# Performance work log

Hardware: AMD Instinct MI355X
Metric: run time of the kernel (lower is better)

## Reference

```python
import jax, jax.numpy as jnp
import numpy as np

N_QUBITS = 8
DEPTH = 1
INPUT_DIM = 64
HIDDEN = 8  # must equal N_QUBITS
SEQ = 64
BATCH = 256


def _apply_rx(state, wire, ang):
    # state: (B, 2, 2, ..., 2) with wire w on axis 1+w; ang: (B,) angles
    n = state.ndim - 1
    st = jnp.moveaxis(state, 1 + wire, -1)
    a0, a1 = st[..., 0], st[..., 1]
    half = ang * 0.5
    c = jnp.cos(half).reshape((-1,) + (1,) * (n - 1))
    s = jnp.sin(half).reshape((-1,) + (1,) * (n - 1))
    new = jnp.stack([c * a0 - 1j * s * a1, c * a1 - 1j * s * a0], axis=-1)
    return jnp.moveaxis(new, -1, 1 + wire)


def _apply_cnot(state, cw, tw):
    st = jnp.moveaxis(state, (1 + cw, 1 + tw), (-2, -1))
    st = st.at[..., 1, :].set(st[..., 1, ::-1])  # flip target where control=1
    return jnp.moveaxis(st, (-2, -1), (1 + cw, 1 + tw))


def qgate(theta, qparams):
    # theta: (B, n) data-dependent RX angles; qparams: (n,) trainable RX angles
    B, n = theta.shape
    state = jnp.zeros((B,) + (2,) * n, dtype=jnp.complex64)
    state = state.at[(slice(None),) + (0,) * n].set(1.0 + 0.0j)  # |0...0>
    for w in range(n):
        state = _apply_rx(state, w, theta[:, w])
    for w in range(n - 1):
        state = _apply_cnot(state, w, w + 1)
    for w in range(n):
        state = _apply_rx(state, w, jnp.broadcast_to(qparams[w], (B,)))
    probs = jnp.abs(state) ** 2  # (B, 2, ..., 2)
    expz = []
    for w in range(n):
        pw = probs.sum(axis=tuple(a for a in range(1, n + 1) if a != 1 + w))  # (B, 2)
        expz.append(pw[:, 0] - pw[:, 1])  # <Z_w>
    return jnp.stack(expz, axis=1)  # (B, n)


def setup_inputs() -> dict:
    key = jax.random.key(0)
    ks = jax.random.split(key, 13)
    d_in = INPUT_DIM + HIDDEN
    d_out = N_QUBITS * DEPTH
    sc = 1.0 / np.sqrt(d_in)
    inp = {"inputs": jax.random.normal(ks[0], (SEQ, BATCH, INPUT_DIM), dtype=jnp.float32)}
    names = ["f", "i", "g", "o"]
    for j, nm in enumerate(names):
        inp["W" + nm] = jax.random.uniform(ks[1 + 3 * j], (d_out, d_in), minval=-sc, maxval=sc, dtype=jnp.float32)
        inp["b" + nm] = jax.random.uniform(ks[2 + 3 * j], (d_out,), minval=-sc, maxval=sc, dtype=jnp.float32)
        inp["q" + nm] = jax.random.normal(ks[3 + 3 * j], (d_out,), dtype=jnp.float32)
    return inp


def reference(inputs, Wf, bf, qf, Wi, bi, qi, Wg, bg, qg, Wo, bo, qo):
    B = inputs.shape[1]
    hx0 = jnp.zeros((B, HIDDEN), dtype=inputs.dtype)
    cx0 = jnp.zeros((B, HIDDEN), dtype=inputs.dtype)

    def step(carry, x_t):
        hx, cx = carry
        comb = jnp.concatenate([x_t, hx], axis=1)  # (B, input+hidden)
        f = jax.nn.sigmoid(qgate(comb @ Wf.T + bf, qf))
        i_ = jax.nn.sigmoid(qgate(comb @ Wi.T + bi, qi))
        g = jnp.tanh(qgate(comb @ Wg.T + bg, qg))
        o = jax.nn.sigmoid(qgate(comb @ Wo.T + bo, qo))
        cx = f * cx + i_ * g
        hx = o * jnp.tanh(cx)
        return (hx, cx), hx

    (hx, cx), outputs = jax.lax.scan(step, (hx0, cx0), inputs)
    return outputs, (hx, cx)
```

## Files before the change

### kernel.cpp

```cpp
#include <hip/hip_runtime.h>
#include <hip/hip_bf16.h>

__device__ float g_pre_static[8 * 1024 * 1024];

__device__ __forceinline__ float rcp_(float x)   { return __builtin_amdgcn_rcpf(x); }
__device__ __forceinline__ float sigm_f(float x) { return rcp_(1.0f + __expf(-x)); }
__device__ __forceinline__ float tanh_f(float x) { return 1.0f - 2.0f*rcp_(__expf(2.0f*x) + 1.0f); }
__device__ __forceinline__ float sigm(float x)  { return 1.0f/(1.0f + __expf(-x)); }
__device__ __forceinline__ float tanh_(float x) { float e = __expf(2.0f*x); return (e-1.0f)/(e+1.0f); }

template<int IDD>
__global__ __launch_bounds__(64) void k_pre8(
    const float* __restrict__ x_,
    const float* __restrict__ W0, const float* __restrict__ b0p,
    const float* __restrict__ W1, const float* __restrict__ b1p,
    const float* __restrict__ W2, const float* __restrict__ b2p,
    const float* __restrict__ W3, const float* __restrict__ b3p,
    float* __restrict__ pre, int S, int B)
{
    constexpr int DIN = IDD + 8;
    __shared__ float wsh[32 * IDD];
    __shared__ float sb32[32];
    const int t   = blockIdx.x;
    const int tid = threadIdx.x;
    const long b  = (long)blockIdx.y * 64 + tid;
    const float* Wp[4] = {W0, W1, W2, W3};
    const float* bp[4] = {b0p, b1p, b2p, b3p};

    #pragma unroll
    for (int it = 0; it < (32*IDD)/64; ++it) {
        int idx = it*64 + tid;
        int gw = idx / IDD, k = idx % IDD;
        wsh[idx] = Wp[gw >> 3][(gw & 7)*DIN + k];
    }
    if (tid < 32) sb32[tid] = bp[tid >> 3][tid & 7];
    __syncthreads();

    if (b >= B) return;
    float xr[IDD];
    const float4* xv = (const float4*)(x_ + ((long)t*B + b)*IDD);
    #pragma unroll
    for (int i = 0; i < IDD/4; ++i) {
        float4 v = xv[i];
        xr[4*i] = v.x; xr[4*i+1] = v.y; xr[4*i+2] = v.z; xr[4*i+3] = v.w;
    }

    float acc[32];
    #pragma unroll
    for (int gw = 0; gw < 32; ++gw) {
        float a = sb32[gw];
        const float4* wr = (const float4*)&wsh[gw*IDD];
        #pragma unroll
        for (int k4 = 0; k4 < IDD/4; ++k4) {
            float4 wv = wr[k4];
            a += xr[4*k4]*wv.x + xr[4*k4+1]*wv.y + xr[4*k4+2]*wv.z + xr[4*k4+3]*wv.w;
        }
        acc[gw] = a;
    }
    float4* op = (float4*)(pre + ((long)t*B + b)*32);
    #pragma unroll
    for (int i = 0; i < 8; ++i)
        op[i] = make_float4(acc[4*i], acc[4*i+1], acc[4*i+2], acc[4*i+3]);
}

__global__ __launch_bounds__(256) void k_pre_gen(
    const float* __restrict__ x_,
    const float* W0, const float* b0p,
    const float* W1, const float* b1p,
    const float* W2, const float* b2p,
    const float* W3, const float* b3p,
    float* __restrict__ pre,
    int S, int B, int ID, int H, int SP)
{
    extern __shared__ float lds[];
    const int dIn  = ID + H;
    const int dInP = dIn + 1;
    float* xs    = lds;
    float* wsh   = lds + 64*SP;
    float* sbias = wsh + 4*H*dInP;
    const int t   = blockIdx.x;
    const int tid = threadIdx.x;
    const int bl  = tid & 63;
    const int q   = tid >> 6;
    const int b0  = blockIdx.y * 64;
    const float* Wp[4] = {W0, W1, W2, W3};
    const float* bp[4] = {b0p, b1p, b2p, b3p};

    for (int g = 0; g < 4; ++g)
        for (int idx = tid; idx < H*dIn; idx += 256) {
            int w = idx / dIn, k = idx - w*dIn;
            wsh[(g*H + w)*dInP + k] = Wp[g][idx];
        }
    for (int idx = tid; idx < 4*H; idx += 256)
        sbias[idx] = bp[idx / H][idx % H];

    {
        int total = 64 * ID;
        for (int i = tid; i < total; i += 256) {
            int r = i / ID, c = i - r*ID;
            long bb = (long)b0 + r; if (bb >= B) bb = B - 1;
            xs[r*SP + c] = x_[((long)t*B + bb)*ID + c];
        }
    }
    __syncthreads();

    const int b = b0 + bl;
    if (b < B) {
        const float* xrow = &xs[bl*SP];
        float* orow = pre + (((long)t*B + b)*4 + q)*H;
        for (int w = 0; w < H; ++w) {
            float acc = sbias[q*H + w];
            const float* wrow = &wsh[(q*H + w)*dInP];
            for (int k = 0; k < ID; ++k) acc += xrow[k] * wrow[k];
            orow[w] = acc;
        }
    }
}

__global__ __launch_bounds__(64) void k_rec8(
    const float* __restrict__ W0, const float* __restrict__ q0,
    const float* __restrict__ W1, const float* __restrict__ q1,
    const float* __restrict__ W2, const float* __restrict__ q2,
    const float* __restrict__ W3, const float* __restrict__ q3,
    const float* __restrict__ pre,
    float* __restrict__ out, int S, int B, int ID)
{
    const int dIn  = ID + 8;
    const int lane = threadIdx.x;
    const int gw   = lane & 31;
    const int g    = gw >> 3;
    const int w    = gw & 7;
    const int b    = blockIdx.x*2 + (lane >> 5);
    const int bs   = (b < B) ? b : (B - 1);
    const float* Wp[4] = {W0, W1, W2, W3};
    const float* qp[4] = {q0, q1, q2, q3};

    float wr[8];
    #pragma unroll
    for (int j = 0; j < 8; ++j) wr[j] = Wp[g][(long)w*dIn + ID + j];
    const float qv   = qp[g][w];
    const float mult = (w < 7) ? __cosf(qv) : 1.0f;
    const float qadd = (w == 7) ? qv : 0.0f;
    const float ascl = (g == 2) ? 2.0f : 1.0f;
    const float aoff = (g == 2) ? -1.0f : 0.0f;

    int oct = lane & 56;
    int srcw[8];
    #pragma unroll
    for (int j = 0; j < 8; ++j) srcw[j] = oct | j;
    int srcg[4];
    #pragma unroll
    for (int G = 0; G < 4; ++G) srcg[G] = (lane & 32) | (G << 3) | w;

    float cxw = 0.0f, hxw = 0.0f;
    float hxj[8];
    #pragma unroll
    for (int j = 0; j < 8; ++j) hxj[j] = 0.0f;

    const float* base = pre + (long)bs*32 + gw;
    const long  tstep = (long)B*32;

    float pf[4];
    #pragma unroll
    for (int d = 0; d < 4; ++d) {
        int tt = (d < S) ? d : (S - 1);
        pf[d] = base[(long)tt*tstep];
    }

    for (int t0 = 0; t0 < S; t0 += 4) {
        #pragma unroll
        for (int d = 0; d < 4; ++d) {
            const int t = t0 + d;
            if (t < S) {
                float pcur = pf[d];
                int tn = t + 4; if (tn >= S) tn = S - 1;
                pf[d] = base[(long)tn*tstep];

                float th = pcur;
                #pragma unroll
                for (int j = 0; j < 8; ++j) th = fmaf(wr[j], hxj[j], th);
                float c = __cosf(th + qadd);

                float cj[8];
                #pragma unroll
                for (int j = 0; j < 8; ++j) cj[j] = __shfl(c, srcw[j], 64);
                float P = cj[0];
                #pragma unroll
                for (int j = 1; j < 8; ++j) P *= (j <= w) ? cj[j] : 1.0f;

                float act = ascl * sigm_f(ascl * (mult * P)) + aoff;

                float fv = __shfl(act, srcg[0], 64);
                float iv = __shfl(act, srcg[1], 64);
                float gv = __shfl(act, srcg[2], 64);
                float ov = __shfl(act, srcg[3], 64);

                cxw = fv*cxw + iv*gv;
                hxw = ov * tanh_f(cxw);

                if (g == 0 && b < B) out[((long)t*B + b)*8 + w] = hxw;

                #pragma unroll
                for (int j = 0; j < 8; ++j) hxj[j] = __shfl(hxw, srcw[j], 64);
            }
        }
    }

    if (g == 0 && b < B) {
        out[((long)S*B + b)*8 + w]     = hxw;
        out[((long)S*B + B + b)*8 + w] = cxw;
    }
}

__global__ __launch_bounds__(64) void k_rec_g(
    const float* __restrict__ pre,
    const float* W0, const float* q0,
    const float* W1, const float* q1,
    const float* W2, const float* q2,
    const float* W3, const float* q3,
    float* __restrict__ out, int S, int B, int ID, int H)
{
    __shared__ float sWh[4*32*32];
    __shared__ float scq[4*32];
    const int dIn = ID + H;
    const int tid = threadIdx.x;
    const int b   = blockIdx.x*64 + tid;
    const float* Wp[4] = {W0, W1, W2, W3};
    const float* qp[4] = {q0, q1, q2, q3};

    for (int idx = tid; idx < 4*H*H; idx += 64) {
        int g = idx / (H*H), r = idx % (H*H);
        int w = r / H, j = r % H;
        sWh[(g*H + w)*H + j] = Wp[g][(long)w*dIn + ID + j];
    }
    for (int idx = tid; idx < 4*H; idx += 64) {
        int g = idx / H, w = idx % H;
        float qv = qp[g][w];
        scq[idx] = (w < H-1) ? __cosf(qv) : qv;
    }
    __syncthreads();
    if (b >= B) return;

    float hx[32], cx[32], gate[4][32], th[32];
    for (int w = 0; w < H; ++w) { hx[w] = 0.0f; cx[w] = 0.0f; }

    for (int t = 0; t < S; ++t) {
        const float* pt = pre + ((long)t*B + b)*4*H;
        for (int g = 0; g < 4; ++g) {
            for (int w = 0; w < H; ++w) {
                float a = pt[g*H + w];
                const float* wrp = &sWh[(g*H + w)*H];
                for (int j = 0; j < H; ++j) a += wrp[j]*hx[j];
                th[w] = a;
            }
            float cum = 1.0f;
            for (int w = 0; w < H-1; ++w) {
                cum *= __cosf(th[w]);
                gate[g][w] = scq[g*H + w] * cum;
            }
            gate[g][H-1] = cum * __cosf(th[H-1] + scq[g*H + H-1]);
        }
        float* orow = out + ((long)t*B + b)*H;
        for (int w = 0; w < H; ++w) {
            float fv = sigm (gate[0][w]);
            float iv = sigm (gate[1][w]);
            float gv = tanh_(gate[2][w]);
            float ov = sigm (gate[3][w]);
            cx[w] = fv*cx[w] + iv*gv;
            hx[w] = ov*tanh_(cx[w]);
            orow[w] = hx[w];
        }
    }
    float* oh = out + ((long)S*B + b)*H;
    float* oc = out + ((long)S*B + B + b)*H;
    for (int w = 0; w < H; ++w) { oh[w] = hx[w]; oc[w] = cx[w]; }
}

static bool derive(long sz[13], long osz, long& S, long& B, long& ID, long& H) {
    H = sz[3];
    long dIn = (H > 0) ? sz[1] / H : 0;
    ID = dIn - H;
    long TB = (ID > 0) ? sz[0] / ID : 0;
    B = (H > 0) ? (osz / H - TB) / 2 : 0;
    S = (B > 0) ? TB / B : 0;
    return (H >= 1 && H <= 32 && ID >= 1 && B >= 1 && S >= 1 &&
            S*B == TB && (S*B + 2*B)*H == osz &&
            dIn*H == sz[1] && TB*ID == sz[0]);
}

extern "C" void kernel_launch(void* const* d_in, const int* in_sizes, int n_in,
                              void* d_out, int out_size, void* d_ws, size_t ws_size,
                              hipStream_t stream) {
    const float* x  = (const float*)d_in[0];
    const float* Wf = (const float*)d_in[1];  const float* bfv = (const float*)d_in[2];  const float* qf = (const float*)d_in[3];
    const float* Wi = (const float*)d_in[4];  const float* biv = (const float*)d_in[5];  const float* qi = (const float*)d_in[6];
    const float* Wg = (const float*)d_in[7];  const float* bgv = (const float*)d_in[8];  const float* qg = (const float*)d_in[9];
    const float* Wo = (const float*)d_in[10]; const float* bov = (const float*)d_in[11]; const float* qo = (const float*)d_in[12];
    float* out = (float*)d_out;

    long S = 0, B = 0, ID = 0, H = 0;
    bool ok = false;
    for (int scale : {1, 4, 2}) {
        long sz[13];
        for (int i = 0; i < 13; ++i) sz[i] = (long)in_sizes[i] / scale;
        long osz = (long)out_size / scale;
        if (derive(sz, osz, S, B, ID, H)) { ok = true; break; }
    }
    if (!ok) { H = 8; ID = 64; B = 256; S = 64; }
    long dIn = ID + H;

    size_t pre_bytes = (size_t)S * 4 * H * B * sizeof(float);
    float* pre = (ws_size >= pre_bytes) ? (float*)d_ws : g_pre_static;

    if (H == 8 && ID == 64) {
        k_pre8<64><<<dim3((unsigned)S, (unsigned)((B + 63) / 64)), dim3(64), 0, stream>>>(
            x, Wf, bfv, Wi, biv, Wg, bgv, Wo, bov, pre, (int)S, (int)B);
    } else {
        int SP = (int)ID + 1;
        size_t lds_bytes = (size_t)(64*SP + 4*H*(dIn + 1) + 4*H) * sizeof(float);
        k_pre_gen<<<dim3((unsigned)S, (unsigned)((B + 63) / 64)), dim3(256), lds_bytes, stream>>>(
            x, Wf, bfv, Wi, biv, Wg, bgv, Wo, bov, pre,
            (int)S, (int)B, (int)ID, (int)H, SP);
    }

    if (H == 8) {
        k_rec8<<<dim3((unsigned)((B + 1) / 2)), dim3(64), 0, stream>>>(
            Wf, qf, Wi, qi, Wg, qg, Wo, qo, pre, out, (int)S, (int)B, (int)ID);
    } else {
        k_rec_g<<<dim3((unsigned)((B + 63) / 64)), dim3(64), 0, stream>>>(
            pre, Wf, qf, Wi, qi, Wg, qg, Wo, qo, out, (int)S, (int)B, (int)ID, (int)H);
    }
}
```

Baseline: 120.6 us.

## Pack two gates per lane in recurrent kernel and use DPP row ops

Each lane of the recurrent kernel now computes two gates for one hidden wire, so a 64-lane wave covers four batch elements instead of two. The cross-lane shuffles for the prefix product, the gate exchange and the hidden-state broadcast are replaced by DPP row shift, row mirror and row rotate operations. The precompute kernel reorders its output so each lane can load its two gate pre-activations as one float2. The aim is to cut shuffle (ds_bpermute) latency on the serial time-step chain and to halve the number of waves. In exchange each lane does twice the FMA and cos work, and the H==8 recurrent path now runs only when ID==64.

```diff
diff --git a/kernel.cpp b/kernel.cpp
--- a/kernel.cpp
+++ b/kernel.cpp
@@ -8,6 +8,12 @@
 __device__ __forceinline__ float tanh_f(float x) { return 1.0f - 2.0f*rcp_(__expf(2.0f*x) + 1.0f); }
 __device__ __forceinline__ float sigm(float x)  { return 1.0f/(1.0f + __expf(-x)); }
 __device__ __forceinline__ float tanh_(float x) { float e = __expf(2.0f*x); return (e-1.0f)/(e+1.0f); }
+
+template<int CTRL>
+__device__ __forceinline__ float dppf(float x) {
+    return __int_as_float(__builtin_amdgcn_update_dpp(
+        0, __float_as_int(x), CTRL, 0xF, 0xF, true));
+}
 
 template<int IDD>
 __global__ __launch_bounds__(64) void k_pre8(
@@ -59,8 +65,12 @@
     }
     float4* op = (float4*)(pre + ((long)t*B + b)*32);
     #pragma unroll
-    for (int i = 0; i < 8; ++i)
-        op[i] = make_float4(acc[4*i], acc[4*i+1], acc[4*i+2], acc[4*i+3]);
+    for (int i = 0; i < 8; ++i) {
+        #define SRC(o) (((((o) >> 4)*2 + ((o) & 1))*8) + ((((o) & 15)) >> 1))
+        op[i] = make_float4(acc[SRC(4*i)], acc[SRC(4*i+1)],
+                            acc[SRC(4*i+2)], acc[SRC(4*i+3)]);
+        #undef SRC
+    }
 }
 
 __global__ __launch_bounds__(256) void k_pre_gen(
@@ -127,40 +137,38 @@
 {
     const int dIn  = ID + 8;
     const int lane = threadIdx.x;
-    const int gw   = lane & 31;
-    const int g    = gw >> 3;
-    const int w    = gw & 7;
-    const int b    = blockIdx.x*2 + (lane >> 5);
+    const int w    = lane & 7;
+    const int gp   = (lane >> 3) & 1;
+    const int b    = blockIdx.x*4 + (lane >> 4);
     const int bs   = (b < B) ? b : (B - 1);
     const float* Wp[4] = {W0, W1, W2, W3};
     const float* qp[4] = {q0, q1, q2, q3};
-
-    float wr[8];
-    #pragma unroll
-    for (int j = 0; j < 8; ++j) wr[j] = Wp[g][(long)w*dIn + ID + j];
-    const float qv   = qp[g][w];
-    const float mult = (w < 7) ? __cosf(qv) : 1.0f;
-    const float qadd = (w == 7) ? qv : 0.0f;
-    const float ascl = (g == 2) ? 2.0f : 1.0f;
-    const float aoff = (g == 2) ? -1.0f : 0.0f;
-
-    int oct = lane & 56;
-    int srcw[8];
-    #pragma unroll
-    for (int j = 0; j < 8; ++j) srcw[j] = oct | j;
-    int srcg[4];
-    #pragma unroll
-    for (int G = 0; G < 4; ++G) srcg[G] = (lane & 32) | (G << 3) | w;
+    const int g0 = 2*gp, g1 = 2*gp + 1;
+
+    float wrot0[8], wrot1[8];
+    #pragma unroll
+    for (int k = 0; k < 8; ++k) {
+        int j = (w - k) & 7;
+        wrot0[k] = Wp[g0][(long)w*dIn + ID + j];
+        wrot1[k] = Wp[g1][(long)w*dIn + ID + j];
+    }
+    const float qv0 = qp[g0][w], qv1 = qp[g1][w];
+    const float mult0 = (w < 7) ? __cosf(qv0) : 1.0f;
+    const float mult1 = (w < 7) ? __cosf(qv1) : 1.0f;
+    const float qadd0 = (w == 7) ? qv0 : 0.0f;
+    const float qadd1 = (w == 7) ? qv1 : 0.0f;
+    const float ascl = gp ? 2.0f : 1.0f;
+    const float aoff = gp ? -1.0f : 0.0f;
 
     float cxw = 0.0f, hxw = 0.0f;
-    float hxj[8];
-    #pragma unroll
-    for (int j = 0; j < 8; ++j) hxj[j] = 0.0f;
-
-    const float* base = pre + (long)bs*32 + gw;
-    const long  tstep = (long)B*32;
-
-    float pf[4];
+    float hxr[8];
+    #pragma unroll
+    for (int k = 0; k < 8; ++k) hxr[k] = 0.0f;
+
+    const float2* base = (const float2*)(pre + (long)bs*32 + gp*16 + 2*w);
+    const long tstep = (long)B*16;
+
+    float2 pf[4];
     #pragma unroll
     for (int d = 0; d < 4; ++d) {
         int tt = (d < S) ? d : (S - 1);
@@ -172,41 +180,55 @@
         for (int d = 0; d < 4; ++d) {
             const int t = t0 + d;
             if (t < S) {
-                float pcur = pf[d];
+                float2 pc = pf[d];
                 int tn = t + 4; if (tn >= S) tn = S - 1;
                 pf[d] = base[(long)tn*tstep];
 
-                float th = pcur;
+                float th0 = pc.x, th1 = pc.y;
                 #pragma unroll
-                for (int j = 0; j < 8; ++j) th = fmaf(wr[j], hxj[j], th);
-                float c = __cosf(th + qadd);
-
-                float cj[8];
-                #pragma unroll
-                for (int j = 0; j < 8; ++j) cj[j] = __shfl(c, srcw[j], 64);
-                float P = cj[0];
-                #pragma unroll
-                for (int j = 1; j < 8; ++j) P *= (j <= w) ? cj[j] : 1.0f;
-
-                float act = ascl * sigm_f(ascl * (mult * P)) + aoff;
-
-                float fv = __shfl(act, srcg[0], 64);
-                float iv = __shfl(act, srcg[1], 64);
-                float gv = __shfl(act, srcg[2], 64);
-                float ov = __shfl(act, srcg[3], 64);
+                for (int k = 0; k < 8; ++k) {
+                    th0 = fmaf(wrot0[k], hxr[k], th0);
+                    th1 = fmaf(wrot1[k], hxr[k], th1);
+                }
+                float P0 = __cosf(th0 + qadd0);
+                float P1 = __cosf(th1 + qadd1);
+
+                float s;
+                s = dppf<0x111>(P0); P0 *= (w >= 1) ? s : 1.0f;
+                s = dppf<0x111>(P1); P1 *= (w >= 1) ? s : 1.0f;
+                s = dppf<0x112>(P0); P0 *= (w >= 2) ? s : 1.0f;
+                s = dppf<0x112>(P1); P1 *= (w >= 2) ? s : 1.0f;
+                s = dppf<0x114>(P0); P0 *= (w >= 4) ? s : 1.0f;
+                s = dppf<0x114>(P1); P1 *= (w >= 4) ? s : 1.0f;
+
+                float act0 = ascl * sigm_f(ascl * (mult0 * P0)) + aoff;
+                float act1 = sigm_f(mult1 * P1);
+
+                float ex0 = dppf<0x128>(act0);
+                float ex1 = dppf<0x128>(act1);
+                float fv = gp ? ex0  : act0;
+                float iv = gp ? ex1  : act1;
+                float gv = gp ? act0 : ex0;
+                float ov = gp ? act1 : ex1;
 
                 cxw = fv*cxw + iv*gv;
                 hxw = ov * tanh_f(cxw);
 
-                if (g == 0 && b < B) out[((long)t*B + b)*8 + w] = hxw;
-
-                #pragma unroll
-                for (int j = 0; j < 8; ++j) hxj[j] = __shfl(hxw, srcw[j], 64);
+                if (gp == 0 && b < B) out[((long)t*B + b)*8 + w] = hxw;
+
+                hxr[0] = hxw;
+                hxr[1] = dppf<0x121>(hxw);
+                hxr[2] = dppf<0x122>(hxw);
+                hxr[3] = dppf<0x123>(hxw);
+                hxr[4] = dppf<0x124>(hxw);
+                hxr[5] = dppf<0x125>(hxw);
+                hxr[6] = dppf<0x126>(hxw);
+                hxr[7] = dppf<0x127>(hxw);
             }
         }
     }
 
-    if (g == 0 && b < B) {
+    if (gp == 0 && b < B) {
         out[((long)S*B + b)*8 + w]     = hxw;
         out[((long)S*B + B + b)*8 + w] = cxw;
     }
@@ -315,18 +337,14 @@
     if (H == 8 && ID == 64) {
         k_pre8<64><<<dim3((unsigned)S, (unsigned)((B + 63) / 64)), dim3(64), 0, stream>>>(
             x, Wf, bfv, Wi, biv, Wg, bgv, Wo, bov, pre, (int)S, (int)B);
+        k_rec8<<<dim3((unsigned)((B + 3) / 4)), dim3(64), 0, stream>>>(
+            Wf, qf, Wi, qi, Wg, qg, Wo, qo, pre, out, (int)S, (int)B, (int)ID);
     } else {
         int SP = (int)ID + 1;
         size_t lds_bytes = (size_t)(64*SP + 4*H*(dIn + 1) + 4*H) * sizeof(float);
         k_pre_gen<<<dim3((unsigned)S, (unsigned)((B + 63) / 64)), dim3(256), lds_bytes, stream>>>(
             x, Wf, bfv, Wi, biv, Wg, bgv, Wo, bov, pre,
             (int)S, (int)B, (int)ID, (int)H, SP);
-    }
-
-    if (H == 8) {
-        k_rec8<<<dim3((unsigned)((B + 1) / 2)), dim3(64), 0, stream>>>(
-            Wf, qf, Wi, qi, Wg, qg, Wo, qo, pre, out, (int)S, (int)B, (int)ID);
-    } else {
         k_rec_g<<<dim3((unsigned)((B + 63) / 64)), dim3(64), 0, stream>>>(
             pre, Wf, qf, Wi, qi, Wg, qg, Wo, qo, out, (int)S, (int)B, (int)ID, (int)H);
     }
```

After: 111.8 us. -7.3%, faster.
